# Kernel optimization log

Measured on AMD Instinct MI355X. Metric: run time of the kernel, lower is better.

The kernel has to match this reference:

```python
import jax, jax.numpy as jnp
import numpy as np

N_NODES = 100000
N_EDGES = 1600000
IN_FEATS = 128
HIDDEN = 128
N_CLASSES = 40
EPS = 1e-5  # BatchNorm1d default eps


def setup_inputs():
    key = jax.random.key(0)
    ks = jax.random.split(key, 12)
    s_in = 1.0 / np.sqrt(IN_FEATS)
    s_h = 1.0 / np.sqrt(HIDDEN)
    return {
        "feat": jax.random.normal(ks[0], (N_NODES, IN_FEATS), jnp.float32),
        "src": jax.random.randint(ks[1], (N_EDGES,), 0, N_NODES, jnp.int32),
        "dst": jax.random.randint(ks[2], (N_EDGES,), 0, N_NODES, jnp.int32),
        # GraphConv weights, stored (out, in) as in the torch module
        "w0": jax.random.normal(ks[3], (HIDDEN, IN_FEATS), jnp.float32) * s_in,
        "w1": jax.random.normal(ks[4], (HIDDEN, HIDDEN), jnp.float32) * s_h,
        "w2": jax.random.normal(ks[5], (N_CLASSES, HIDDEN), jnp.float32) * s_h,
        "b2": jnp.zeros((N_CLASSES,), jnp.float32),  # bias only on last layer
        # skip-connection linears (use_linear=True, bias=False)
        "l0": jax.random.normal(ks[6], (HIDDEN, IN_FEATS), jnp.float32) * s_in,
        "l1": jax.random.normal(ks[7], (HIDDEN, HIDDEN), jnp.float32) * s_h,
        "l2": jax.random.normal(ks[8], (N_CLASSES, HIDDEN), jnp.float32) * s_h,
        # BatchNorm affine params for the two hidden layers
        "g0": jnp.ones((HIDDEN,), jnp.float32),
        "beta0": jnp.zeros((HIDDEN,), jnp.float32),
        "g1": jnp.ones((HIDDEN,), jnp.float32),
        "beta1": jnp.zeros((HIDDEN,), jnp.float32),
    }


def _spmm(h, src, dst):
    # copy_u + sum aggregation: out[d] = sum_{e: dst[e]==d} h[src[e]]
    return jax.ops.segment_sum(h[src], dst, num_segments=N_NODES)


def gcn_forward(feat, src, dst, w0, w1, w2, b2, l0, l1, l2, g0, beta0, g1, beta1):
    ones = jnp.ones((src.shape[0],), jnp.float32)
    out_deg = jnp.clip(jax.ops.segment_sum(ones, src, num_segments=N_NODES), 1.0)
    in_deg = jnp.clip(jax.ops.segment_sum(ones, dst, num_segments=N_NODES), 1.0)
    out_norm = out_deg ** -0.5  # norm='both', applied to src features
    in_norm = in_deg ** -0.5    # norm='both', applied to aggregated result

    def conv(h, W, bias, in_gt_out):
        hs = h * out_norm[:, None]
        if in_gt_out:  # in_feats > out_feats: project first, then aggregate
            rst = _spmm(hs @ W.T, src, dst)
        else:          # aggregate first, then project
            rst = _spmm(hs, src, dst) @ W.T
        rst = rst * in_norm[:, None]
        if bias is not None:
            rst = rst + bias
        return rst

    def bn(x, g, b):
        mu = x.mean(0)
        var = x.var(0)  # biased variance, matches BN training-mode normalization
        return (x - mu) * jax.lax.rsqrt(var + EPS) * g + b

    h = feat  # dropout in eval mode = identity
    h = jax.nn.relu(bn(conv(h, w0, None, IN_FEATS > HIDDEN) + h @ l0.T, g0, beta0))
    h = jax.nn.relu(bn(conv(h, w1, None, False) + h @ l1.T, g1, beta1))
    h = conv(h, w2, b2, HIDDEN > N_CLASSES) + h @ l2.T
    return h


def reference(feat, src, dst, w0, w1, w2, b2, l0, l1, l2, g0, beta0, g1, beta1):
    return gcn_forward(feat, src, dst, w0, w1, w2, b2, l0, l1, l2, g0, beta0, g1, beta1)
```

## Files before the change

### kernel.cpp

```cpp
#include <hip/hip_runtime.h>
#include <hip/hip_fp16.h>
#include <cstdint>
#include <cstddef>

#define N_NODES 100000
#define N_EDGES 1600000
#define EPS 1e-5f

typedef _Float16 half8 __attribute__((ext_vector_type(8)));
typedef float floatx4 __attribute__((ext_vector_type(4)));

#define HCH 64
#define HRG 4
#define HBINS 32768
#define HWORDS (HBINS / 2)
#define HCHUNK (N_EDGES / HCH)
#define HCHUNK4 (HCHUNK / 4)

__global__ void k_hist_part(const int* __restrict__ keys, unsigned int* __restrict__ Hpart) {
  __shared__ unsigned int bins[HWORDS];
  int c = blockIdx.x % HCH, r = blockIdx.x / HCH;
  int base = r * HBINS;
  for (int i = threadIdx.x; i < HWORDS; i += 256) bins[i] = 0;
  __syncthreads();
  const int4* k4 = (const int4*)(keys + c * HCHUNK);
  for (int i = threadIdx.x; i < HCHUNK4; i += 256) {
    int4 k = k4[i];
    int a;
    a = k.x - base; if ((unsigned)a < (unsigned)HBINS) atomicAdd(&bins[a >> 1], 1u << ((a & 1) * 16));
    a = k.y - base; if ((unsigned)a < (unsigned)HBINS) atomicAdd(&bins[a >> 1], 1u << ((a & 1) * 16));
    a = k.z - base; if ((unsigned)a < (unsigned)HBINS) atomicAdd(&bins[a >> 1], 1u << ((a & 1) * 16));
    a = k.w - base; if ((unsigned)a < (unsigned)HBINS) atomicAdd(&bins[a >> 1], 1u << ((a & 1) * 16));
  }
  __syncthreads();
  unsigned int* outp = Hpart + ((size_t)blockIdx.x << 14);
  for (int i = threadIdx.x; i < HWORDS; i += 256) outp[i] = bins[i];
}

__global__ void k_hist_sum(const unsigned short* __restrict__ Hp, int* __restrict__ deg) {
  int b = blockIdx.x * 256 + threadIdx.x;
  if (b >= N_NODES) return;
  int r = b >> 15, lo = b & (HBINS - 1);
  const unsigned short* p = Hp + ((size_t)(r * HCH) << 15) + lo;
  unsigned int t = 0;
#pragma unroll 8
  for (int c = 0; c < HCH; ++c) t += p[(size_t)c << 15];
  deg[b] = (int)t;
}

__global__ void k_hist_scan(unsigned short* __restrict__ Hp, const int* __restrict__ degs,
                            int* __restrict__ degd, float* __restrict__ out_norm,
                            float* __restrict__ in_norm, int* __restrict__ bsum) {
  __shared__ int sred[256];
  int t = threadIdx.x;
  int b = blockIdx.x * 256 + t;
  int total = 0;
  if (b < N_NODES) {
    int r = b >> 15, lo = b & (HBINS - 1);
    unsigned short* p = Hp + ((size_t)(r * HCH) << 15) + lo;
    unsigned int tt = 0;
#pragma unroll 8
    for (int c = 0; c < HCH; ++c) {
      unsigned int v = p[(size_t)c << 15];
      p[(size_t)c << 15] = (unsigned short)tt;
      tt += v;
    }
    total = (int)tt;
    degd[b] = total;
    out_norm[b] = rsqrtf((float)max(degs[b], 1));
    in_norm[b] = rsqrtf((float)max(total, 1));
  }
  sred[t] = total;
  __syncthreads();
  for (int off = 128; off > 0; off >>= 1) {
    if (t < off) sred[t] += sred[t + off];
    __syncthreads();
  }
  if (t == 0) bsum[blockIdx.x] = sred[0];
}

__global__ void k_build(const int* __restrict__ src, const int* __restrict__ dst,
                        const unsigned short* __restrict__ Hbase,
                        const int* __restrict__ row_start, int* __restrict__ col) {
  __shared__ unsigned int cur[HWORDS];
  int c = blockIdx.x % HCH, r = blockIdx.x / HCH;
  int base = r * HBINS;
  for (int i = threadIdx.x; i < HWORDS; i += 256) cur[i] = 0;
  __syncthreads();
  const unsigned short* hb = Hbase + ((size_t)blockIdx.x << 15);
  const int4* d4 = (const int4*)(dst + c * HCHUNK);
  const int4* s4 = (const int4*)(src + c * HCHUNK);
  for (int i = threadIdx.x; i < HCHUNK4; i += 256) {
    int4 d = d4[i];
    int4 s = s4[i];
    int a;
    a = d.x - base;
    if ((unsigned)a < (unsigned)HBINS) {
      unsigned old = atomicAdd(&cur[a >> 1], 1u << ((a & 1) * 16));
      unsigned lr = (old >> ((a & 1) * 16)) & 0xffffu;
      col[row_start[d.x] + hb[a] + lr] = s.x;
    }
    a = d.y - base;
    if ((unsigned)a < (unsigned)HBINS) {
      unsigned old = atomicAdd(&cur[a >> 1], 1u << ((a & 1) * 16));
      unsigned lr = (old >> ((a & 1) * 16)) & 0xffffu;
      col[row_start[d.y] + hb[a] + lr] = s.y;
    }
    a = d.z - base;
    if ((unsigned)a < (unsigned)HBINS) {
      unsigned old = atomicAdd(&cur[a >> 1], 1u << ((a & 1) * 16));
      unsigned lr = (old >> ((a & 1) * 16)) & 0xffffu;
      col[row_start[d.z] + hb[a] + lr] = s.z;
    }
    a = d.w - base;
    if ((unsigned)a < (unsigned)HBINS) {
      unsigned old = atomicAdd(&cur[a >> 1], 1u << ((a & 1) * 16));
      unsigned lr = (old >> ((a & 1) * 16)) & 0xffffu;
      col[row_start[d.w] + hb[a] + lr] = s.w;
    }
  }
}

__global__ void k_scan2(int* bsum, int nb) {
  __shared__ int s[512];
  int t = threadIdx.x;
  int v = (t < nb) ? bsum[t] : 0;
  s[t] = v;
  __syncthreads();
  for (int off = 1; off < 512; off <<= 1) {
    int x = (t >= off) ? s[t - off] : 0;
    __syncthreads();
    s[t] += x;
    __syncthreads();
  }
  if (t < nb) bsum[t] = s[t] - v;
}

__global__ void k_scan3(const int* __restrict__ degd, const int* __restrict__ bsum,
                        int* row_start) {
  __shared__ int s[256];
  int t = threadIdx.x;
  int i = blockIdx.x * 256 + t;
  int v = (i < N_NODES) ? degd[i] : 0;
  s[t] = v;
  __syncthreads();
  for (int off = 1; off < 256; off <<= 1) {
    int x = (t >= off) ? s[t - off] : 0;
    __syncthreads();
    s[t] += x;
    __syncthreads();
  }
  if (i < N_NODES) row_start[i] = bsum[blockIdx.x] + s[t] - v;
  if (i == 0) row_start[N_NODES] = N_EDGES;
}

__global__ void k_w2h(const float* __restrict__ w0, const float* __restrict__ l0,
                      const float* __restrict__ w1, const float* __restrict__ l1,
                      const float* __restrict__ w2, const float* __restrict__ l2,
                      unsigned short* __restrict__ W) {
  int i = blockIdx.x * 256 + threadIdx.x;
  if (i >= 18944) return;
  int h = i * 4;
  const float* src; int off;
  if (h < 16384)      { src = w0; off = h; }
  else if (h < 32768) { src = l0; off = h - 16384; }
  else if (h < 49152) { src = w1; off = h - 32768; }
  else if (h < 65536) { src = l1; off = h - 49152; }
  else if (h < 70656) { src = w2; off = h - 65536; }
  else                { src = l2; off = h - 70656; }
  float4 v = *(const float4*)(src + off);
  ushort4 o;
  o.x = __half_as_ushort(__float2half_rn(v.x));
  o.y = __half_as_ushort(__float2half_rn(v.y));
  o.z = __half_as_ushort(__float2half_rn(v.z));
  o.w = __half_as_ushort(__float2half_rn(v.w));
  ((ushort4*)W)[i] = o;
}

__global__ void k_feat2h(const float* __restrict__ feat, unsigned short* __restrict__ F) {
  int i = blockIdx.x * 256 + threadIdx.x;
  if (i >= N_NODES * 32) return;
  float4 v = ((const float4*)feat)[i];
  ushort4 u;
  u.x = __half_as_ushort(__float2half_rn(v.x));
  u.y = __half_as_ushort(__float2half_rn(v.y));
  u.z = __half_as_ushort(__float2half_rn(v.z));
  u.w = __half_as_ushort(__float2half_rn(v.w));
  ((ushort4*)F)[i] = u;
}

__global__ void k_agg128h(const unsigned short* __restrict__ F, const int* __restrict__ col,
                          const int* __restrict__ row_start,
                          const float* __restrict__ out_norm,
                          const float* __restrict__ in_norm,
                          unsigned short* __restrict__ out16) {
  int wave = threadIdx.x >> 6;
  int lane = threadIdx.x & 63;
  int node = blockIdx.x * 4 + wave;
  if (node >= N_NODES) return;
  int q = lane >> 4;
  int sub = lane & 15;
  int s0 = row_start[node], s1 = row_start[node + 1];
  const uint4* hp = (const uint4*)F;
  float a[8];
#pragma unroll
  for (int j = 0; j < 8; ++j) a[j] = 0.f;
  int e = s0 + q;
  for (; e + 4 < s1; e += 8) {
    int c0 = col[e];
    int c1 = col[e + 4];
    float on0 = out_norm[c0];
    float on1 = out_norm[c1];
    uint4 u0 = hp[(size_t)c0 * 16 + sub];
    uint4 u1 = hp[(size_t)c1 * 16 + sub];
    const __half2* h0 = (const __half2*)&u0;
    const __half2* h1 = (const __half2*)&u1;
#pragma unroll
    for (int j = 0; j < 4; ++j) {
      float2 f0 = __half22float2(h0[j]);
      float2 f1 = __half22float2(h1[j]);
      a[2 * j] += on0 * f0.x + on1 * f1.x;
      a[2 * j + 1] += on0 * f0.y + on1 * f1.y;
    }
  }
  if (e < s1) {
    int c = col[e];
    float on = out_norm[c];
    uint4 u = hp[(size_t)c * 16 + sub];
    const __half2* h0 = (const __half2*)&u;
#pragma unroll
    for (int j = 0; j < 4; ++j) {
      float2 f = __half22float2(h0[j]);
      a[2 * j] += on * f.x;
      a[2 * j + 1] += on * f.y;
    }
  }
#pragma unroll
  for (int j = 0; j < 8; ++j) {
    a[j] += __shfl_xor(a[j], 16);
    a[j] += __shfl_xor(a[j], 32);
  }
  if (q == 0) {
    float sc = in_norm[node];
    __half2 o[4];
#pragma unroll
    for (int j = 0; j < 4; ++j)
      o[j] = __float22half2_rn(make_float2(a[2 * j] * sc, a[2 * j + 1] * sc));
    ((uint4*)out16)[(size_t)node * 16 + sub] = *(const uint4*)o;
  }
}

__launch_bounds__(256)
__global__ void k_gemm_dual16(const unsigned short* __restrict__ Xa,
                              const unsigned short* __restrict__ Xh,
                              const unsigned short* __restrict__ W16,
                              unsigned short* __restrict__ Out16, float* __restrict__ pstats) {
  __shared__ __align__(16) unsigned short smem[128 * 136];
  int t = threadIdx.x;
  int row0 = blockIdx.x * 64;
  int w = t >> 6, lane = t & 63;
  int q = lane >> 4, m = lane & 15;
  size_t arow = (size_t)min(row0 + w * 16 + m, N_NODES - 1);
  floatx4 acc[8];
#pragma unroll
  for (int i = 0; i < 8; ++i) acc[i] = (floatx4){0.f, 0.f, 0.f, 0.f};

  for (int phase = 0; phase < 2; ++phase) {
    const unsigned short* Xg = phase ? Xh : Xa;
    const uint4* xr = (const uint4*)Xg + arow * 16 + q;
    uint4 av[4];
    av[0] = xr[0]; av[1] = xr[4]; av[2] = xr[8]; av[3] = xr[12];
    __syncthreads();
    {
      const uint4* wsrc = (const uint4*)(W16 + ((size_t)phase << 14));
#pragma unroll
      for (int it = 0; it < 8; ++it) {
        int idx = it * 256 + t;
        *(uint4*)&smem[(idx >> 4) * 136 + (idx & 15) * 8] = wsrc[idx];
      }
    }
    __syncthreads();
#pragma unroll
    for (int ks = 0; ks < 4; ++ks) {
      half8 a = *(half8*)&av[ks];
      int kk = ks * 32 + q * 8;
#pragma unroll
      for (int t8 = 0; t8 < 8; ++t8) {
        half8 b = *(const half8*)&smem[(t8 * 16 + m) * 136 + kk];
        acc[t8] = __builtin_amdgcn_mfma_f32_16x16x32_f16(a, b, acc[t8], 0, 0, 0);
      }
    }
  }
  float ps[8], pq[8];
#pragma unroll
  for (int t8 = 0; t8 < 8; ++t8) {
    float s = 0.f, sq = 0.f;
#pragma unroll
    for (int i = 0; i < 4; ++i) {
      int row = row0 + w * 16 + q * 4 + i;
      if (row < N_NODES) {
        float v = acc[t8][i];
        s += v; sq += v * v;
      }
    }
    s += __shfl_xor(s, 16);
    s += __shfl_xor(s, 32);
    sq += __shfl_xor(sq, 16);
    sq += __shfl_xor(sq, 32);
    ps[t8] = s; pq[t8] = sq;
  }
  __syncthreads();
  unsigned short* sT = smem;
  float* pSum = (float*)(smem + 8704);
  float* pSq = pSum + 512;
#pragma unroll
  for (int t8 = 0; t8 < 8; ++t8) {
    int c = t8 * 16 + m;
#pragma unroll
    for (int i = 0; i < 4; ++i) {
      int r = w * 16 + q * 4 + i;
      sT[r * 136 + c] = __half_as_ushort(__float2half_rn(acc[t8][i]));
    }
    if (q == 0) {
      pSum[w * 128 + c] = ps[t8];
      pSq[w * 128 + c] = pq[t8];
    }
  }
  __syncthreads();
#pragma unroll
  for (int it = 0; it < 4; ++it) {
    int idx = it * 256 + t;
    int r = idx >> 4, g = idx & 15;
    int row = row0 + r;
    if (row < N_NODES)
      *(uint4*)&Out16[(size_t)row * 128 + g * 8] = *(const uint4*)&sT[r * 136 + g * 8];
  }
  if (t < 128) {
    float s = (pSum[t] + pSum[128 + t]) + (pSum[256 + t] + pSum[384 + t]);
    float sq = (pSq[t] + pSq[128 + t]) + (pSq[256 + t] + pSq[384 + t]);
    pstats[(size_t)blockIdx.x * 256 + t] = s;
    pstats[(size_t)blockIdx.x * 256 + 128 + t] = sq;
  }
}

__global__ void k_stats_red(const float* __restrict__ pstats, float* __restrict__ stats,
                            int nblk) {
  int t = threadIdx.x;
  float s = 0.f;
  for (int b = blockIdx.x; b < nblk; b += gridDim.x)
    s += pstats[(size_t)b * 256 + t];
  atomicAdd(&stats[t], s);
}

__global__ void k_bnrelu16(const unsigned short* __restrict__ x16,
                           const float* __restrict__ stats,
                           const float* __restrict__ g, const float* __restrict__ b,
                           unsigned short* __restrict__ F) {
  __shared__ float sc[128], sh[128];
  int t = threadIdx.x;
  if (t < 128) {
    const float inv = 1.f / (float)N_NODES;
    float mu = stats[t] * inv;
    float var = stats[128 + t] * inv - mu * mu;
    float rs = rsqrtf(var + EPS);
    float s = rs * g[t];
    sc[t] = s;
    sh[t] = b[t] - mu * s;
  }
  __syncthreads();
  int i = blockIdx.x * 256 + t;
  if (i >= N_NODES * 16) return;
  int c8 = (i & 15) * 8;
  uint4 raw = ((const uint4*)x16)[i];
  const __half2* hp2 = (const __half2*)&raw;
  float v[8];
#pragma unroll
  for (int j = 0; j < 4; ++j) {
    float2 f = __half22float2(hp2[j]);
    v[2 * j] = f.x;
    v[2 * j + 1] = f.y;
  }
#pragma unroll
  for (int j = 0; j < 8; ++j) {
    float y = v[j] * sc[c8 + j] + sh[c8 + j];
    v[j] = y > 0.f ? y : 0.f;
  }
  ushort4 o[2];
#pragma unroll
  for (int j = 0; j < 8; ++j) ((unsigned short*)o)[j] = __half_as_ushort(__float2half_rn(v[j]));
  ((uint4*)F)[i] = *(const uint4*)o;
}

__launch_bounds__(256)
__global__ void k_gemm2_16(const unsigned short* __restrict__ X,
                           const unsigned short* __restrict__ W80,
                           const float* __restrict__ b2,
                           const float* __restrict__ out_norm,
                           __half* __restrict__ p, float* __restrict__ out) {
  __shared__ __align__(16) unsigned short smem[80 * 136];
  int t = threadIdx.x;
  int row0 = blockIdx.x * 64;
  int w = t >> 6, lane = t & 63;
  int q = lane >> 4, m = lane & 15;
  size_t arow = (size_t)min(row0 + w * 16 + m, N_NODES - 1);
  const uint4* xr = (const uint4*)X + arow * 16 + q;
  uint4 av[4];
  av[0] = xr[0]; av[1] = xr[4]; av[2] = xr[8]; av[3] = xr[12];
  {
    const uint4* wsrc = (const uint4*)W80;
#pragma unroll
    for (int it = 0; it < 5; ++it) {
      int idx = it * 256 + t;
      *(uint4*)&smem[(idx >> 4) * 136 + (idx & 15) * 8] = wsrc[idx];
    }
  }
  __syncthreads();
  floatx4 acc[5];
#pragma unroll
  for (int i = 0; i < 5; ++i) acc[i] = (floatx4){0.f, 0.f, 0.f, 0.f};
#pragma unroll
  for (int ks = 0; ks < 4; ++ks) {
    half8 a = *(half8*)&av[ks];
    int kk = ks * 32 + q * 8;
#pragma unroll
    for (int t5 = 0; t5 < 5; ++t5) {
      half8 b = *(const half8*)&smem[(t5 * 16 + m) * 136 + kk];
      acc[t5] = __builtin_amdgcn_mfma_f32_16x16x32_f16(a, b, acc[t5], 0, 0, 0);
    }
  }
  __syncthreads();
  unsigned short* sTp = smem;
  float* sTo = (float*)(smem + 4608);
  {
    unsigned int* zp = (unsigned int*)sTp;
    for (int idx = t; idx < 768; idx += 256) {
      int r = idx / 12, wc = 20 + idx % 12;
      zp[r * 36 + wc] = 0u;
    }
  }
  float on4[4];
#pragma unroll
  for (int i = 0; i < 4; ++i) {
    int row = row0 + w * 16 + q * 4 + i;
    on4[i] = out_norm[min(row, N_NODES - 1)];
  }
#pragma unroll
  for (int t5 = 0; t5 < 5; ++t5) {
    int c = t5 * 16 + m;
#pragma unroll
    for (int i = 0; i < 4; ++i) {
      int r = w * 16 + q * 4 + i;
      if (c < 40) {
        sTp[r * 72 + c] = __half_as_ushort(__float2half_rn(on4[i] * acc[t5][i]));
      } else {
        sTo[r * 44 + (c - 40)] = acc[t5][i] + b2[c - 40];
      }
    }
  }
  __syncthreads();
#pragma unroll
  for (int it = 0; it < 2; ++it) {
    int idx = it * 256 + t;
    int r = idx >> 3, g = idx & 7;
    int row = row0 + r;
    if (row < N_NODES)
      *(uint4*)((unsigned short*)p + (size_t)row * 64 + g * 8) = *(const uint4*)&sTp[r * 72 + g * 8];
  }
  for (int it = 0; it < 3; ++it) {
    int idx = it * 256 + t;
    if (idx < 640) {
      int r = idx / 10, g = idx % 10;
      int row = row0 + r;
      if (row < N_NODES)
        *(float4*)(out + (size_t)row * 40 + g * 4) = *(const float4*)&sTo[r * 44 + g * 4];
    }
  }
}

__global__ void k_agg64h(const __half* __restrict__ p, const int* __restrict__ col,
                         const int* __restrict__ row_start,
                         const float* __restrict__ in_norm,
                         float* __restrict__ out) {
  int wave = threadIdx.x >> 6, lane = threadIdx.x & 63;
  int node = blockIdx.x * 4 + wave;
  if (node >= N_NODES) return;
  int oct = lane >> 3;
  int sub = lane & 7;
  int s0 = row_start[node], s1 = row_start[node + 1];
  const uint4* pp = (const uint4*)p;
  float a[8];
#pragma unroll
  for (int j = 0; j < 8; ++j) a[j] = 0.f;
  int e = s0 + oct;
  for (; e + 8 < s1; e += 16) {
    int c0 = col[e];
    int c1 = col[e + 8];
    uint4 u0 = pp[(size_t)c0 * 8 + sub];
    uint4 u1 = pp[(size_t)c1 * 8 + sub];
    const __half2* h0 = (const __half2*)&u0;
    const __half2* h1 = (const __half2*)&u1;
#pragma unroll
    for (int j = 0; j < 4; ++j) {
      float2 f0 = __half22float2(h0[j]);
      float2 f1 = __half22float2(h1[j]);
      a[2 * j] += f0.x + f1.x;
      a[2 * j + 1] += f0.y + f1.y;
    }
  }
  if (e < s1) {
    uint4 u = pp[(size_t)col[e] * 8 + sub];
    const __half2* h0 = (const __half2*)&u;
#pragma unroll
    for (int j = 0; j < 4; ++j) {
      float2 f = __half22float2(h0[j]);
      a[2 * j] += f.x;
      a[2 * j + 1] += f.y;
    }
  }
#pragma unroll
  for (int j = 0; j < 8; ++j) {
    a[j] += __shfl_xor(a[j], 8);
    a[j] += __shfl_xor(a[j], 16);
    a[j] += __shfl_xor(a[j], 32);
  }
  if (oct == 0 && sub < 5) {
    float sc = in_norm[node];
    float4* op = (float4*)(out + (size_t)node * 40 + (size_t)sub * 8);
    float4 v0 = op[0], v1 = op[1];
    v0.x += sc * a[0]; v0.y += sc * a[1]; v0.z += sc * a[2]; v0.w += sc * a[3];
    v1.x += sc * a[4]; v1.y += sc * a[5]; v1.z += sc * a[6]; v1.w += sc * a[7];
    op[0] = v0; op[1] = v1;
  }
}

extern "C" void kernel_launch(void* const* d_in, const int* in_sizes, int n_in,
                              void* d_out, int out_size, void* d_ws, size_t ws_size,
                              hipStream_t stream) {
  const float* feat = (const float*)d_in[0];
  const int* src = (const int*)d_in[1];
  const int* dst = (const int*)d_in[2];
  const float* w0 = (const float*)d_in[3];
  const float* w1 = (const float*)d_in[4];
  const float* w2 = (const float*)d_in[5];
  const float* b2 = (const float*)d_in[6];
  const float* l0 = (const float*)d_in[7];
  const float* l1 = (const float*)d_in[8];
  const float* l2 = (const float*)d_in[9];
  const float* g0 = (const float*)d_in[10];
  const float* beta0 = (const float*)d_in[11];
  const float* g1 = (const float*)d_in[12];
  const float* beta1 = (const float*)d_in[13];
  float* out = (float*)d_out;

  char* ws = (char*)d_ws;
  size_t off = 0;
  auto alloc = [&](size_t bytes) {
    void* ptr = ws + off;
    off = (off + bytes + 255) & ~(size_t)255;
    return ptr;
  };
  unsigned short* A16 = (unsigned short*)alloc(2 * (size_t)N_NODES * 128);
  float* B = (float*)alloc(sizeof(float) * (size_t)N_NODES * 128);
  unsigned short* F = (unsigned short*)alloc(2 * (size_t)N_NODES * 128);
  int* degs = (int*)alloc(sizeof(int) * N_NODES);
  int* degd = (int*)alloc(sizeof(int) * N_NODES);
  int* row_start = (int*)alloc(sizeof(int) * (N_NODES + 1));
  int* colb = (int*)alloc(sizeof(int) * N_EDGES);
  float* out_norm = (float*)alloc(sizeof(float) * N_NODES);
  float* in_norm = (float*)alloc(sizeof(float) * N_NODES);
  int* bsum = (int*)alloc(sizeof(int) * 512);
  float* stats = (float*)alloc(sizeof(float) * 256);
  unsigned short* W16 = (unsigned short*)alloc(2 * (size_t)75776);
  int gb = (N_NODES + 63) / 64;
  float* pstats = (float*)alloc(sizeof(float) * (size_t)gb * 256);

  unsigned int* Hpart = (unsigned int*)B;
  unsigned short* B16 = (unsigned short*)B;

  int nb = (N_NODES + 255) / 256;
  int hb = HCH * HRG;

  k_w2h<<<74, 256, 0, stream>>>(w0, l0, w1, l1, w2, l2, W16);

  k_hist_part<<<hb, 256, 0, stream>>>(src, Hpart);
  k_hist_sum<<<nb, 256, 0, stream>>>((const unsigned short*)Hpart, degs);
  k_hist_part<<<hb, 256, 0, stream>>>(dst, Hpart);
  k_hist_scan<<<nb, 256, 0, stream>>>((unsigned short*)Hpart, degs, degd,
                                      out_norm, in_norm, bsum);
  k_scan2<<<1, 512, 0, stream>>>(bsum, nb);
  k_scan3<<<nb, 256, 0, stream>>>(degd, bsum, row_start);
  k_build<<<hb, 256, 0, stream>>>(src, dst, (const unsigned short*)Hpart, row_start, colb);

  int ab = (N_NODES + 3) / 4;
  int fb = (N_NODES * 32 + 255) / 256;
  int hb16 = (N_NODES * 16 + 255) / 256;

  k_feat2h<<<fb, 256, 0, stream>>>(feat, F);
  k_agg128h<<<ab, 256, 0, stream>>>(F, colb, row_start, out_norm, in_norm, A16);
  k_gemm_dual16<<<gb, 256, 0, stream>>>(A16, F, W16, B16, pstats);
  hipMemsetAsync(stats, 0, sizeof(float) * 256, stream);
  k_stats_red<<<32, 256, 0, stream>>>(pstats, stats, gb);
  k_bnrelu16<<<hb16, 256, 0, stream>>>(B16, stats, g0, beta0, F);

  k_agg128h<<<ab, 256, 0, stream>>>(F, colb, row_start, out_norm, in_norm, A16);
  k_gemm_dual16<<<gb, 256, 0, stream>>>(A16, F, W16 + 32768, B16, pstats);
  hipMemsetAsync(stats, 0, sizeof(float) * 256, stream);
  k_stats_red<<<32, 256, 0, stream>>>(pstats, stats, gb);
  k_bnrelu16<<<hb16, 256, 0, stream>>>(B16, stats, g1, beta1, F);

  __half* p = (__half*)A16;
  k_gemm2_16<<<gb, 256, 0, stream>>>(F, W16 + 65536, b2, out_norm, p, out);
  k_agg64h<<<ab, 256, 0, stream>>>(p, colb, row_start, in_norm, out);
}
```

Baseline: 497.5 us.

## Fuse BatchNorm+ReLU into downstream aggregation and GEMM loads; merge degree histogram kernels

Removes the standalone BN+ReLU kernels by applying the normalization and ReLU on the fly wherever the pre-activation is read: in the gather of the next aggregation, in the skip-branch GEMM operand, and in the final GEMM. The source-degree histogram now gets its own buffer, so its reduction folds into the scan kernel and one launch disappears. This saves a full read-write pass over the 100k x 128 half activations per layer. In exchange the aggregation recomputes the affine+ReLU for every edge gather, and the workspace must hold both histograms.

After: 476.5 us. -4.2%, faster.

```diff
diff --git a/kernel.cpp b/kernel.cpp
--- a/kernel.cpp
+++ b/kernel.cpp
@@ -37,37 +37,31 @@
   for (int i = threadIdx.x; i < HWORDS; i += 256) outp[i] = bins[i];
 }
 
-__global__ void k_hist_sum(const unsigned short* __restrict__ Hp, int* __restrict__ deg) {
-  int b = blockIdx.x * 256 + threadIdx.x;
-  if (b >= N_NODES) return;
-  int r = b >> 15, lo = b & (HBINS - 1);
-  const unsigned short* p = Hp + ((size_t)(r * HCH) << 15) + lo;
-  unsigned int t = 0;
-#pragma unroll 8
-  for (int c = 0; c < HCH; ++c) t += p[(size_t)c << 15];
-  deg[b] = (int)t;
-}
-
-__global__ void k_hist_scan(unsigned short* __restrict__ Hp, const int* __restrict__ degs,
-                            int* __restrict__ degd, float* __restrict__ out_norm,
-                            float* __restrict__ in_norm, int* __restrict__ bsum) {
+__global__ void k_hist_scan2(const unsigned short* __restrict__ Hs,
+                             unsigned short* __restrict__ Hd,
+                             int* __restrict__ degd, float* __restrict__ out_norm,
+                             float* __restrict__ in_norm, int* __restrict__ bsum) {
   __shared__ int sred[256];
   int t = threadIdx.x;
   int b = blockIdx.x * 256 + t;
   int total = 0;
   if (b < N_NODES) {
     int r = b >> 15, lo = b & (HBINS - 1);
-    unsigned short* p = Hp + ((size_t)(r * HCH) << 15) + lo;
+    const unsigned short* ps = Hs + ((size_t)(r * HCH) << 15) + lo;
+    unsigned int ds = 0;
+#pragma unroll 8
+    for (int c = 0; c < HCH; ++c) ds += ps[(size_t)c << 15];
+    unsigned short* pd = Hd + ((size_t)(r * HCH) << 15) + lo;
     unsigned int tt = 0;
 #pragma unroll 8
     for (int c = 0; c < HCH; ++c) {
-      unsigned int v = p[(size_t)c << 15];
-      p[(size_t)c << 15] = (unsigned short)tt;
+      unsigned int v = pd[(size_t)c << 15];
+      pd[(size_t)c << 15] = (unsigned short)tt;
       tt += v;
     }
     total = (int)tt;
     degd[b] = total;
-    out_norm[b] = rsqrtf((float)max(degs[b], 1));
+    out_norm[b] = rsqrtf((float)max((int)ds, 1));
     in_norm[b] = rsqrtf((float)max(total, 1));
   }
   sred[t] = total;
@@ -189,19 +183,40 @@
   ((ushort4*)F)[i] = u;
 }
 
-__global__ void k_agg128h(const unsigned short* __restrict__ F, const int* __restrict__ col,
+template<int BN>
+__global__ void k_agg128h(const unsigned short* __restrict__ X, const int* __restrict__ col,
                           const int* __restrict__ row_start,
                           const float* __restrict__ out_norm,
                           const float* __restrict__ in_norm,
+                          const float* __restrict__ stats,
+                          const float* __restrict__ g, const float* __restrict__ bb,
                           unsigned short* __restrict__ out16) {
-  int wave = threadIdx.x >> 6;
-  int lane = threadIdx.x & 63;
+  __shared__ float scA[128], shA[128];
+  int t = threadIdx.x;
+  if (BN) {
+    if (t < 128) {
+      const float inv = 1.f / (float)N_NODES;
+      float mu = stats[t] * inv;
+      float var = stats[128 + t] * inv - mu * mu;
+      float s = rsqrtf(var + EPS) * g[t];
+      scA[t] = s;
+      shA[t] = bb[t] - mu * s;
+    }
+    __syncthreads();
+  }
+  int wave = t >> 6;
+  int lane = t & 63;
   int node = blockIdx.x * 4 + wave;
   if (node >= N_NODES) return;
   int q = lane >> 4;
   int sub = lane & 15;
+  float scR[8], shR[8];
+  if (BN) {
+#pragma unroll
+    for (int j = 0; j < 8; ++j) { scR[j] = scA[sub * 8 + j]; shR[j] = shA[sub * 8 + j]; }
+  }
   int s0 = row_start[node], s1 = row_start[node + 1];
-  const uint4* hp = (const uint4*)F;
+  const uint4* hp = (const uint4*)X;
   float a[8];
 #pragma unroll
   for (int j = 0; j < 8; ++j) a[j] = 0.f;
@@ -219,6 +234,12 @@
     for (int j = 0; j < 4; ++j) {
       float2 f0 = __half22float2(h0[j]);
       float2 f1 = __half22float2(h1[j]);
+      if (BN) {
+        f0.x = fmaxf(f0.x * scR[2 * j] + shR[2 * j], 0.f);
+        f0.y = fmaxf(f0.y * scR[2 * j + 1] + shR[2 * j + 1], 0.f);
+        f1.x = fmaxf(f1.x * scR[2 * j] + shR[2 * j], 0.f);
+        f1.y = fmaxf(f1.y * scR[2 * j + 1] + shR[2 * j + 1], 0.f);
+      }
       a[2 * j] += on0 * f0.x + on1 * f1.x;
       a[2 * j + 1] += on0 * f0.y + on1 * f1.y;
     }
@@ -231,6 +252,10 @@
 #pragma unroll
     for (int j = 0; j < 4; ++j) {
       float2 f = __half22float2(h0[j]);
+      if (BN) {
+        f.x = fmaxf(f.x * scR[2 * j] + shR[2 * j], 0.f);
+        f.y = fmaxf(f.y * scR[2 * j + 1] + shR[2 * j + 1], 0.f);
+      }
       a[2 * j] += on * f.x;
       a[2 * j + 1] += on * f.y;
     }
@@ -250,16 +275,28 @@
   }
 }
 
+template<int BN>
 __launch_bounds__(256)
 __global__ void k_gemm_dual16(const unsigned short* __restrict__ Xa,
                               const unsigned short* __restrict__ Xh,
+                              const float* __restrict__ stats,
+                              const float* __restrict__ g, const float* __restrict__ bb,
                               const unsigned short* __restrict__ W16,
                               unsigned short* __restrict__ Out16, float* __restrict__ pstats) {
   __shared__ __align__(16) unsigned short smem[128 * 136];
+  __shared__ float scA[128], shA[128];
   int t = threadIdx.x;
   int row0 = blockIdx.x * 64;
   int w = t >> 6, lane = t & 63;
   int q = lane >> 4, m = lane & 15;
+  if (BN && t < 128) {
+    const float inv = 1.f / (float)N_NODES;
+    float mu = stats[t] * inv;
+    float var = stats[128 + t] * inv - mu * mu;
+    float s = rsqrtf(var + EPS) * g[t];
+    scA[t] = s;
+    shA[t] = bb[t] - mu * s;
+  }
   size_t arow = (size_t)min(row0 + w * 16 + m, N_NODES - 1);
   floatx4 acc[8];
 #pragma unroll
@@ -277,6 +314,20 @@
       for (int it = 0; it < 8; ++it) {
         int idx = it * 256 + t;
         *(uint4*)&smem[(idx >> 4) * 136 + (idx & 15) * 8] = wsrc[idx];
+      }
+    }
+    if (BN && phase == 1) {
+#pragma unroll
+      for (int ks = 0; ks < 4; ++ks) {
+        int kk = ks * 32 + q * 8;
+        __half2* hh = (__half2*)&av[ks];
+#pragma unroll
+        for (int j = 0; j < 4; ++j) {
+          float2 f = __half22float2(hh[j]);
+          f.x = fmaxf(f.x * scA[kk + 2 * j] + shA[kk + 2 * j], 0.f);
+          f.y = fmaxf(f.y * scA[kk + 2 * j + 1] + shA[kk + 2 * j + 1], 0.f);
+          hh[j] = __float22half2_rn(f);
+        }
       }
     }
     __syncthreads();
@@ -330,10 +381,10 @@
 #pragma unroll
   for (int it = 0; it < 4; ++it) {
     int idx = it * 256 + t;
-    int r = idx >> 4, g = idx & 15;
+    int r = idx >> 4, gg = idx & 15;
     int row = row0 + r;
     if (row < N_NODES)
-      *(uint4*)&Out16[(size_t)row * 128 + g * 8] = *(const uint4*)&sT[r * 136 + g * 8];
+      *(uint4*)&Out16[(size_t)row * 128 + gg * 8] = *(const uint4*)&sT[r * 136 + gg * 8];
   }
   if (t < 128) {
     float s = (pSum[t] + pSum[128 + t]) + (pSum[256 + t] + pSum[384 + t]);
@@ -352,56 +403,28 @@
   atomicAdd(&stats[t], s);
 }
 
-__global__ void k_bnrelu16(const unsigned short* __restrict__ x16,
-                           const float* __restrict__ stats,
-                           const float* __restrict__ g, const float* __restrict__ b,
-                           unsigned short* __restrict__ F) {
-  __shared__ float sc[128], sh[128];
-  int t = threadIdx.x;
-  if (t < 128) {
-    const float inv = 1.f / (float)N_NODES;
-    float mu = stats[t] * inv;
-    float var = stats[128 + t] * inv - mu * mu;
-    float rs = rsqrtf(var + EPS);
-    float s = rs * g[t];
-    sc[t] = s;
-    sh[t] = b[t] - mu * s;
-  }
-  __syncthreads();
-  int i = blockIdx.x * 256 + t;
-  if (i >= N_NODES * 16) return;
-  int c8 = (i & 15) * 8;
-  uint4 raw = ((const uint4*)x16)[i];
-  const __half2* hp2 = (const __half2*)&raw;
-  float v[8];
-#pragma unroll
-  for (int j = 0; j < 4; ++j) {
-    float2 f = __half22float2(hp2[j]);
-    v[2 * j] = f.x;
-    v[2 * j + 1] = f.y;
-  }
-#pragma unroll
-  for (int j = 0; j < 8; ++j) {
-    float y = v[j] * sc[c8 + j] + sh[c8 + j];
-    v[j] = y > 0.f ? y : 0.f;
-  }
-  ushort4 o[2];
-#pragma unroll
-  for (int j = 0; j < 8; ++j) ((unsigned short*)o)[j] = __half_as_ushort(__float2half_rn(v[j]));
-  ((uint4*)F)[i] = *(const uint4*)o;
-}
-
 __launch_bounds__(256)
 __global__ void k_gemm2_16(const unsigned short* __restrict__ X,
+                           const float* __restrict__ stats,
+                           const float* __restrict__ g, const float* __restrict__ bb,
                            const unsigned short* __restrict__ W80,
                            const float* __restrict__ b2,
                            const float* __restrict__ out_norm,
                            __half* __restrict__ p, float* __restrict__ out) {
   __shared__ __align__(16) unsigned short smem[80 * 136];
+  __shared__ float scA[128], shA[128];
   int t = threadIdx.x;
   int row0 = blockIdx.x * 64;
   int w = t >> 6, lane = t & 63;
   int q = lane >> 4, m = lane & 15;
+  if (t < 128) {
+    const float inv = 1.f / (float)N_NODES;
+    float mu = stats[t] * inv;
+    float var = stats[128 + t] * inv - mu * mu;
+    float s = rsqrtf(var + EPS) * g[t];
+    scA[t] = s;
+    shA[t] = bb[t] - mu * s;
+  }
   size_t arow = (size_t)min(row0 + w * 16 + m, N_NODES - 1);
   const uint4* xr = (const uint4*)X + arow * 16 + q;
   uint4 av[4];
@@ -415,6 +438,18 @@
     }
   }
   __syncthreads();
+#pragma unroll
+  for (int ks = 0; ks < 4; ++ks) {
+    int kk = ks * 32 + q * 8;
+    __half2* hh = (__half2*)&av[ks];
+#pragma unroll
+    for (int j = 0; j < 4; ++j) {
+      float2 f = __half22float2(hh[j]);
+      f.x = fmaxf(f.x * scA[kk + 2 * j] + shA[kk + 2 * j], 0.f);
+      f.y = fmaxf(f.y * scA[kk + 2 * j + 1] + shA[kk + 2 * j + 1], 0.f);
+      hh[j] = __float22half2_rn(f);
+    }
+  }
   floatx4 acc[5];
 #pragma unroll
   for (int i = 0; i < 5; ++i) acc[i] = (floatx4){0.f, 0.f, 0.f, 0.f};
@@ -461,18 +496,18 @@
 #pragma unroll
   for (int it = 0; it < 2; ++it) {
     int idx = it * 256 + t;
-    int r = idx >> 3, g = idx & 7;
+    int r = idx >> 3, gg = idx & 7;
     int row = row0 + r;
     if (row < N_NODES)
-      *(uint4*)((unsigned short*)p + (size_t)row * 64 + g * 8) = *(const uint4*)&sTp[r * 72 + g * 8];
+      *(uint4*)((unsigned short*)p + (size_t)row * 64 + gg * 8) = *(const uint4*)&sTp[r * 72 + gg * 8];
   }
   for (int it = 0; it < 3; ++it) {
     int idx = it * 256 + t;
     if (idx < 640) {
-      int r = idx / 10, g = idx % 10;
+      int r = idx / 10, gg = idx % 10;
       int row = row0 + r;
       if (row < N_NODES)
-        *(float4*)(out + (size_t)row * 40 + g * 4) = *(const float4*)&sTo[r * 44 + g * 4];
+        *(float4*)(out + (size_t)row * 40 + gg * 4) = *(const float4*)&sTo[r * 44 + gg * 4];
     }
   }
 }
@@ -562,53 +597,55 @@
   unsigned short* A16 = (unsigned short*)alloc(2 * (size_t)N_NODES * 128);
   float* B = (float*)alloc(sizeof(float) * (size_t)N_NODES * 128);
   unsigned short* F = (unsigned short*)alloc(2 * (size_t)N_NODES * 128);
-  int* degs = (int*)alloc(sizeof(int) * N_NODES);
   int* degd = (int*)alloc(sizeof(int) * N_NODES);
   int* row_start = (int*)alloc(sizeof(int) * (N_NODES + 1));
   int* colb = (int*)alloc(sizeof(int) * N_EDGES);
   float* out_norm = (float*)alloc(sizeof(float) * N_NODES);
   float* in_norm = (float*)alloc(sizeof(float) * N_NODES);
   int* bsum = (int*)alloc(sizeof(int) * 512);
-  float* stats = (float*)alloc(sizeof(float) * 256);
+  float* stats0 = (float*)alloc(sizeof(float) * 256);
+  float* stats1 = (float*)alloc(sizeof(float) * 256);
   unsigned short* W16 = (unsigned short*)alloc(2 * (size_t)75776);
   int gb = (N_NODES + 63) / 64;
   float* pstats = (float*)alloc(sizeof(float) * (size_t)gb * 256);
 
-  unsigned int* Hpart = (unsigned int*)B;
-  unsigned short* B16 = (unsigned short*)B;
+  unsigned int* Hs = (unsigned int*)B;
+  unsigned int* Hd = Hs + (size_t)HCH * HRG * HWORDS;
+  unsigned short* P0 = (unsigned short*)B;
+  unsigned short* P1 = F;
 
   int nb = (N_NODES + 255) / 256;
   int hb = HCH * HRG;
 
   k_w2h<<<74, 256, 0, stream>>>(w0, l0, w1, l1, w2, l2, W16);
 
-  k_hist_part<<<hb, 256, 0, stream>>>(src, Hpart);
-  k_hist_sum<<<nb, 256, 0, stream>>>((const unsigned short*)Hpart, degs);
-  k_hist_part<<<hb, 256, 0, stream>>>(dst, Hpart);
-  k_hist_scan<<<nb, 256, 0, stream>>>((unsigned short*)Hpart, degs, degd,
-                                      out_norm, in_norm, bsum);
+  k_hist_part<<<hb, 256, 0, stream>>>(src, Hs);
+  k_hist_part<<<hb, 256, 0, stream>>>(dst, Hd);
+  k_hist_scan2<<<nb, 256, 0, stream>>>((const unsigned short*)Hs, (unsigned short*)Hd,
+                                       degd, out_norm, in_norm, bsum);
   k_scan2<<<1, 512, 0, stream>>>(bsum, nb);
   k_scan3<<<nb, 256, 0, stream>>>(degd, bsum, row_start);
-  k_build<<<hb, 256, 0, stream>>>(src, dst, (const unsigned short*)Hpart, row_start, colb);
+  k_build<<<hb, 256, 0, stream>>>(src, dst, (const unsigned short*)Hd, row_start, colb);
 
   int ab = (N_NODES + 3) / 4;
   int fb = (N_NODES * 32 + 255) / 256;
-  int hb16 = (N_NODES * 16 + 255) / 256;
 
   k_feat2h<<<fb, 256, 0, stream>>>(feat, F);
-  k_agg128h<<<ab, 256, 0, stream>>>(F, colb, row_start, out_norm, in_norm, A16);
-  k_gemm_dual16<<<gb, 256, 0, stream>>>(A16, F, W16, B16, pstats);
-  hipMemsetAsync(stats, 0, sizeof(float) * 256, stream);
-  k_stats_red<<<32, 256, 0, stream>>>(pstats, stats, gb);
-  k_bnrelu16<<<hb16, 256, 0, stream>>>(B16, stats, g0, beta0, F);
-
-  k_agg128h<<<ab, 256, 0, stream>>>(F, colb, row_start, out_norm, in_norm, A16);
-  k_gemm_dual16<<<gb, 256, 0, stream>>>(A16, F, W16 + 32768, B16, pstats);
-  hipMemsetAsync(stats, 0, sizeof(float) * 256, stream);
-  k_stats_red<<<32, 256, 0, stream>>>(pstats, stats, gb);
-  k_bnrelu16<<<hb16, 256, 0, stream>>>(B16, stats, g1, beta1, F);
+  k_agg128h<0><<<ab, 256, 0, stream>>>(F, colb, row_start, out_norm, in_norm,
+                                       nullptr, nullptr, nullptr, A16);
+  k_gemm_dual16<0><<<gb, 256, 0, stream>>>(A16, F, nullptr, nullptr, nullptr,
+                                           W16, P0, pstats);
+  hipMemsetAsync(stats0, 0, sizeof(float) * 256, stream);
+  k_stats_red<<<32, 256, 0, stream>>>(pstats, stats0, gb);
+
+  k_agg128h<1><<<ab, 256, 0, stream>>>(P0, colb, row_start, out_norm, in_norm,
+                                       stats0, g0, beta0, A16);
+  k_gemm_dual16<1><<<gb, 256, 0, stream>>>(A16, P0, stats0, g0, beta0,
+                                           W16 + 32768, P1, pstats);
+  hipMemsetAsync(stats1, 0, sizeof(float) * 256, stream);
+  k_stats_red<<<32, 256, 0, stream>>>(pstats, stats1, gb);
 
   __half* p = (__half*)A16;
-  k_gemm2_16<<<gb, 256, 0, stream>>>(F, W16 + 65536, b2, out_norm, p, out);
+  k_gemm2_16<<<gb, 256, 0, stream>>>(P1, stats1, g1, beta1, W16 + 65536, b2, out_norm, p, out);
   k_agg64h<<<ab, 256, 0, stream>>>(p, colb, row_start, in_norm, out);
 }
```
